# Optimization experiments

Hardware: AMD Instinct MI355X
Metric: run time of the kernel (lower is better)

## Reference

```python
import jax, jax.numpy as jnp
import numpy as np

B, N, K = 4, 4096, 16
C_IN = 128
EPS = 1e-5


def setup_inputs() -> dict:
    key = jax.random.key(0)
    ks = jax.random.split(key, 8)
    c0 = 2 * C_IN + 3  # concat channels: pos_diff(3) + feat2(128) + feat1(128)
    return {
        "pos1": jax.random.normal(ks[0], (B, 3, N), jnp.float32),
        "pos2": jax.random.normal(ks[1], (B, 3, N), jnp.float32),
        "feature1": jax.random.normal(ks[2], (B, C_IN, N), jnp.float32),
        "feature2": jax.random.normal(ks[3], (B, C_IN, N), jnp.float32),
        "W0": jax.random.normal(ks[4], (128, c0), jnp.float32) * 0.05,
        "W1": jax.random.normal(ks[5], (128, 128), jnp.float32) * 0.05,
        "W2": jax.random.normal(ks[6], (128, 128), jnp.float32) * 0.05,
        "g0": jnp.ones((128,), jnp.float32),
        "g1": jnp.ones((128,), jnp.float32),
        "g2": jnp.ones((128,), jnp.float32),
        "b0": jnp.zeros((128,), jnp.float32),
        "b1": jnp.zeros((128,), jnp.float32),
        "b2": jnp.zeros((128,), jnp.float32),
    }


def _knn_idx(pos1, pos2, k):
    # pos1, pos2: (B, 3, N).  For each point in pos1, k nearest points in pos2.
    p1 = pos1.transpose(0, 2, 1)  # (B, N, 3)
    p2 = pos2.transpose(0, 2, 1)  # (B, M, 3)
    d = (jnp.sum(p1 * p1, -1, keepdims=True)
         + jnp.sum(p2 * p2, -1)[:, None, :]
         - 2.0 * jnp.einsum("bnc,bmc->bnm", p1, p2))  # (B, N, M) squared dists
    _, idx = jax.lax.top_k(-d, k)  # (B, N, K)
    return idx


def _group(x, idx):
    # x: (B, C, M), idx: (B, N, K) -> (B, C, N, K)
    xt = x.transpose(0, 2, 1)  # (B, M, C)
    g = jax.vmap(lambda a, i: a[i])(xt, idx)  # (B, N, K, C)
    return g.transpose(0, 3, 1, 2)


def _conv_bn_relu(x, W, g, b):
    # 1x1 conv (no bias) + BatchNorm2d (training: batch stats, biased var) + ReLU
    y = jnp.einsum("oc,bcnk->bonk", W, x)
    mu = jnp.mean(y, axis=(0, 2, 3), keepdims=True)
    var = jnp.var(y, axis=(0, 2, 3), keepdims=True)
    yn = (y - mu) * jax.lax.rsqrt(var + EPS)
    return jax.nn.relu(yn * g[None, :, None, None] + b[None, :, None, None])


def reference(pos1, pos2, feature1, feature2, W0, W1, W2, g0, g1, g2, b0, b1, b2):
    idx = _knn_idx(pos1, pos2, K)                      # (B, N, K)
    pos2_g = _group(pos2, idx)                         # (B, 3, N, K)
    pos_diff = pos2_g - pos1[:, :, :, None]
    feat2_g = _group(feature2, idx)                    # (B, C, N, K)
    feat1_rep = jnp.broadcast_to(feature1[:, :, :, None], (B, C_IN, N, K))
    x = jnp.concatenate([pos_diff, feat2_g, feat1_rep], axis=1)  # (B, 2C+3, N, K)
    x = _conv_bn_relu(x, W0, g0, b0)
    x = _conv_bn_relu(x, W1, g1, b1)
    x = _conv_bn_relu(x, W2, g2, b2)
    feat1_new = jnp.max(x, axis=-1)                    # (B, mlp[-1], N)
    return (pos1, feat1_new)
```

## Files before the change

kernel.cpp:

```cpp
#include <hip/hip_runtime.h>

#define B_ 4
#define N_ 4096
#define K_ 16
#define C_ 128
#define NQ (B_*N_)
#define COLS_TOT (NQ*K_)
#define CNT_F 262144.0f
#define EPS_ 1e-5f

typedef __attribute__((ext_vector_type(8))) short short8;
typedef __attribute__((ext_vector_type(4))) float f4;
typedef __attribute__((ext_vector_type(4))) int i4;
typedef unsigned long long u64;

__device__ __forceinline__ unsigned short f2bf(float f){
  unsigned u = __builtin_bit_cast(unsigned, f);
  u = u + 0x7fffu + ((u >> 16) & 1u);
  return (unsigned short)(u >> 16);
}
__device__ __forceinline__ float bf2f(unsigned short h){
  return __builtin_bit_cast(float, ((unsigned)h) << 16);
}
__device__ __forceinline__ int swzc(int c){ return c ^ ((c >> 3) & 7); }

__global__ __launch_bounds__(256) void wconv(
    const float* __restrict__ W0, const float* __restrict__ W1, const float* __restrict__ W2,
    unsigned short* __restrict__ W0b, unsigned short* __restrict__ W0c,
    unsigned short* __restrict__ W1b, unsigned short* __restrict__ W2b)
{
  int i = blockIdx.x * 256 + threadIdx.x;
  int sel = i >> 14, r = i & 16383;
  int o = r >> 7, c = r & 127;
  float v; unsigned short* dst;
  if (sel == 0)      { v = W0[o*259 + 3   + c]; dst = W0b; }
  else if (sel == 1) { v = W0[o*259 + 131 + c]; dst = W0c; }
  else if (sel == 2) { v = W1[o*128 + c];       dst = W1b; }
  else               { v = W2[o*128 + c];       dst = W2b; }
  dst[r] = f2bf(v);
}

__global__ __launch_bounds__(256) void knn_chunk(
    const float* __restrict__ pos1, const float* __restrict__ pos2,
    u64* __restrict__ kout)
{
  __shared__ __align__(16) float pts[256*4];
  int bx = blockIdx.x;
  int b = bx >> 8, rest = bx & 255, ngrp = rest >> 4, chunk = rest & 15;
  int t = threadIdx.x;
  int m0 = chunk * 256;
  const float* p2 = pos2 + (size_t)b*3*N_;
  {
    int m = m0 + t;
    float x = p2[m], y = p2[N_ + m], z = p2[2*N_ + m];
    float sq = __fadd_rn(__fadd_rn(__fmul_rn(x,x), __fmul_rn(y,y)), __fmul_rn(z,z));
    f4 v; v.x = x; v.y = y; v.z = z; v.w = sq;
    *(f4*)(pts + t*4) = v;
  }
  __syncthreads();

  int n = ngrp*256 + t;
  const float* p1 = pos1 + (size_t)b*3*N_;
  float qx = p1[n], qy = p1[N_ + n], qz = p1[2*N_ + n];
  float qs = __fadd_rn(__fadd_rn(__fmul_rn(qx,qx), __fmul_rn(qy,qy)), __fmul_rn(qz,qz));

  u64 list[16];
  #pragma unroll
  for (int j = 0; j < 16; ++j) list[j] = ~0ull;

  #pragma unroll 1
  for (int tile = 0; tile < 16; ++tile){
    u64 tk[16];
    #pragma unroll
    for (int e = 0; e < 16; ++e){
      int it = tile*16 + e;
      f4 c = *(const f4*)(pts + it*4);
      float dot = __builtin_fmaf(qz, c.z,
                    __builtin_fmaf(qy, c.y, __fmul_rn(qx, c.x)));
      float d = __fsub_rn(__fadd_rn(qs, c.w), __fmul_rn(2.0f, dot));
      d = __fadd_rn(d, 0.0f);
      unsigned u = __builtin_bit_cast(unsigned, d);
      u ^= (unsigned)((int)u >> 31) | 0x80000000u;
      tk[e] = ((u64)u << 12) | (unsigned)(m0 + it);
    }
    #pragma unroll
    for (int k = 2; k <= 16; k <<= 1)
      #pragma unroll
      for (int j2 = k >> 1; j2 > 0; j2 >>= 1)
        #pragma unroll
        for (int i = 0; i < 16; ++i){
          int l = i ^ j2;
          if (l > i){
            bool up = ((i & k) == 0);
            u64 a = tk[i], bb = tk[l];
            bool sw = up ? (a > bb) : (a < bb);
            u64 lo = sw ? bb : a, hi = sw ? a : bb;
            tk[i] = lo; tk[l] = hi;
          }
        }
    u64 m16[16];
    #pragma unroll
    for (int i = 0; i < 16; ++i){
      u64 a = list[i], bb = tk[15 - i];
      m16[i] = a < bb ? a : bb;
    }
    #pragma unroll
    for (int j2 = 8; j2 > 0; j2 >>= 1)
      #pragma unroll
      for (int i = 0; i < 16; ++i){
        int l = i ^ j2;
        if (l > i){
          u64 a = m16[i], bb = m16[l];
          bool sw = a > bb;
          m16[i] = sw ? bb : a; m16[l] = sw ? a : bb;
        }
      }
    #pragma unroll
    for (int i = 0; i < 16; ++i) list[i] = m16[i];
  }

  int q = b*N_ + n;
  #pragma unroll
  for (int j = 0; j < 16; ++j)
    kout[(size_t)(chunk*16 + j)*NQ + q] = list[j];
}

__global__ __launch_bounds__(256) void knn_merge(
    const u64* __restrict__ kin, int* __restrict__ idxout)
{
  int q = blockIdx.x*256 + threadIdx.x;
  u64 list[16];
  #pragma unroll
  for (int j = 0; j < 16; ++j) list[j] = ~0ull;
  #pragma unroll 1
  for (int l = 0; l < 16; ++l){
    u64 lv[16];
    #pragma unroll
    for (int j = 0; j < 16; ++j)
      lv[j] = kin[(size_t)(l*16 + j)*NQ + q];
    bool dead = false;
    #pragma unroll
    for (int j = 0; j < 16; ++j){
      bool ins = !dead && (list[15] > lv[j]);
      dead = !ins;
      if (__any(ins)){
        if (ins){
          u64 key = lv[j];
          bool cm = list[14] > key;
          list[15] = cm ? list[14] : key;
          #pragma unroll
          for (int jj = 14; jj >= 1; --jj){
            bool cj = cm;
            cm = list[jj-1] > key;
            list[jj] = cj ? (cm ? list[jj-1] : key) : list[jj];
          }
          list[0] = cm ? key : list[0];
        }
      }
    }
  }
  #pragma unroll
  for (int j = 0; j < 4; ++j){
    i4 v;
    v.x = (int)(list[j*4]   & 0xFFF); v.y = (int)(list[j*4+1] & 0xFFF);
    v.z = (int)(list[j*4+2] & 0xFFF); v.w = (int)(list[j*4+3] & 0xFFF);
    *(i4*)(idxout + (size_t)q*16 + j*4) = v;
  }
}

__global__ __launch_bounds__(256) void p1_gemm(
    const float* __restrict__ feat2, const float* __restrict__ feat1,
    const unsigned short* __restrict__ W0b, const unsigned short* __restrict__ W0c,
    float* __restrict__ F2t, float* __restrict__ PREt)
{
  __shared__ __align__(16) unsigned short X[16*128*8];
  int bid = blockIdx.x;
  int sel = bid >> 7;
  const float* src = sel ? feat1 : feat2;
  const unsigned short* W = sel ? W0c : W0b;
  float* dst = sel ? PREt : F2t;
  int c0 = (bid & 127) * 128;
  int b = c0 >> 12, mm0 = c0 & 4095;
  int t = threadIdx.x;
  {
    int colt = t & 127, chh = t >> 7;
    #pragma unroll 4
    for (int it = 0; it < 64; ++it){
      int ch = it*2 + chh;
      float v = src[((size_t)b*C_ + ch)*N_ + mm0 + colt];
      X[(ch >> 3)*1024 + swzc(colt)*8 + (ch & 7)] = f2bf(v);
    }
  }
  int lane = t & 63, w = t >> 6;
  int or0 = (w >> 1)*64, c0w = (w & 1)*64;
  int lr = lane & 15, lg = lane >> 4;
  short8 af[4][4];
  #pragma unroll
  for (int ks = 0; ks < 4; ++ks)
    #pragma unroll
    for (int i = 0; i < 4; ++i)
      af[ks][i] = *(const short8*)(W + (or0 + 16*i + lr)*128 + ks*32 + 8*lg);
  __syncthreads();

  f4 acc[4][4] = {};
  #pragma unroll
  for (int ks = 0; ks < 4; ++ks){
    short8 bfr[4];
    #pragma unroll
    for (int j = 0; j < 4; ++j)
      bfr[j] = *(const short8*)(X + (ks*4 + lg)*1024 + swzc(c0w + 16*j + lr)*8);
    #pragma unroll
    for (int i = 0; i < 4; ++i)
      #pragma unroll
      for (int j = 0; j < 4; ++j)
        acc[i][j] = __builtin_amdgcn_mfma_f32_16x16x32_bf16(af[ks][i], bfr[j], acc[i][j], 0, 0, 0);
  }
  #pragma unroll
  for (int i = 0; i < 4; ++i)
    #pragma unroll
    for (int j = 0; j < 4; ++j){
      int col = c0 + c0w + 16*j + lr;
      *(f4*)(dst + (size_t)col*C_ + or0 + 16*i + 4*lg) = acc[i][j];
    }
}

__global__ __launch_bounds__(256) void k3_stats(
    const float* __restrict__ pos1, const float* __restrict__ pos2,
    const float* __restrict__ W0, const int* __restrict__ idx,
    const float* __restrict__ F2t, const float* __restrict__ PREt,
    float* __restrict__ partials)
{
  __shared__ float w0a[384];
  __shared__ float ldsS[256];
  int t = threadIdx.x;
  for (int i = t; i < 384; i += 256) w0a[i] = W0[(i/3)*259 + (i%3)];
  __syncthreads();
  int cloc = t & 15, chg = t >> 4, ch0 = chg*8;
  float wx[8], wy[8], wz[8];
  #pragma unroll
  for (int e = 0; e < 8; ++e){
    wx[e] = w0a[(ch0+e)*3]; wy[e] = w0a[(ch0+e)*3+1]; wz[e] = w0a[(ch0+e)*3+2];
  }
  float s1[8] = {}, s2[8] = {};
  int base = blockIdx.x * 256;
  for (int it = 0; it < 16; ++it){
    int col = base + it*16 + cloc;
    int nabs = col >> 4;
    int b = nabs >> 12, n = nabs & 4095;
    int m = idx[col];
    float dx = pos2[(size_t)(b*3+0)*N_ + m] - pos1[(size_t)(b*3+0)*N_ + n];
    float dy = pos2[(size_t)(b*3+1)*N_ + m] - pos1[(size_t)(b*3+1)*N_ + n];
    float dz = pos2[(size_t)(b*3+2)*N_ + m] - pos1[(size_t)(b*3+2)*N_ + n];
    const float* f2 = F2t  + ((size_t)b*N_ + m)*C_ + ch0;
    const float* pr = PREt + ((size_t)b*N_ + n)*C_ + ch0;
    #pragma unroll
    for (int e = 0; e < 8; ++e){
      float y = f2[e] + pr[e];
      y = fmaf(wx[e], dx, y); y = fmaf(wy[e], dy, y); y = fmaf(wz[e], dz, y);
      s1[e] += y; s2[e] = fmaf(y, y, s2[e]);
    }
  }
  #pragma unroll
  for (int e = 0; e < 8; ++e){
    float a = s1[e], q = s2[e];
    #pragma unroll
    for (int sft = 1; sft < 16; sft <<= 1){ a += __shfl_xor(a, sft); q += __shfl_xor(q, sft); }
    if (cloc == 0){ ldsS[ch0 + e] = a; ldsS[128 + ch0 + e] = q; }
  }
  __syncthreads();
  partials[(size_t)blockIdx.x*256 + t] = ldsS[t];
}

__global__ __launch_bounds__(256) void reduce1(const float* __restrict__ partials,
                                               float* __restrict__ partial2)
{
  int t = threadIdx.x, r0 = blockIdx.x*32;
  float a = 0.f;
  #pragma unroll 4
  for (int i = 0; i < 32; ++i) a += partials[(size_t)(r0+i)*256 + t];
  partial2[(size_t)blockIdx.x*256 + t] = a;
}

__global__ __launch_bounds__(256) void finalize(const float* __restrict__ partial2, int rows,
    const float* __restrict__ g, const float* __restrict__ bb,
    float* __restrict__ cA, float* __restrict__ cB)
{
  __shared__ float sh[256];
  int t = threadIdx.x;
  float a = 0.f;
  for (int i = 0; i < rows; ++i) a += partial2[(size_t)i*256 + t];
  sh[t] = a;
  __syncthreads();
  if (t < 128){
    float mu = sh[t] / CNT_F;
    float var = sh[128 + t] / CNT_F - mu*mu;
    float A = g[t] * rsqrtf(var + EPS_);
    cA[t] = A; cB[t] = bb[t] - mu*A;
  }
}

__global__ __launch_bounds__(256,2) void layer1_fused(
    const float* __restrict__ pos1, const float* __restrict__ pos2,
    const float* __restrict__ W0, const int* __restrict__ idx,
    const float* __restrict__ F2t, const float* __restrict__ PREt,
    unsigned short* __restrict__ ybuf,
    const unsigned short* __restrict__ Wbf,
    const float* __restrict__ cA, const float* __restrict__ cB,
    float* __restrict__ partials)
{
  __shared__ __align__(16) char lds[40960];
  unsigned short* X = (unsigned short*)lds;
  float* ldsA = (float*)(lds + 32768);
  float* ldsB = ldsA + 128;
  float* w0a  = ldsB + 128;
  float* ldsS = w0a + 384;
  int t = threadIdx.x;
  int c0 = blockIdx.x * 128;
  if (t < 128){ ldsA[t] = cA[t]; ldsB[t] = cB[t]; }
  for (int i = t; i < 384; i += 256) w0a[i] = W0[(i/3)*259 + (i%3)];
  ldsS[t] = 0.f; ldsS[256 + t] = 0.f;
  __syncthreads();

  int lane = t & 63, w = t >> 6;
  int or0 = (w >> 1)*64, c0w = (w & 1)*64;
  int lr = lane & 15, lg = lane >> 4;

  {
    int colL = t >> 1, half = t & 1;
    int col = c0 + colL;
    int nabs = col >> 4;
    int b = nabs >> 12, n = nabs & 4095;
    int m = idx[col];
    float dx = pos2[(size_t)(b*3+0)*N_ + m] - pos1[(size_t)(b*3+0)*N_ + n];
    float dy = pos2[(size_t)(b*3+1)*N_ + m] - pos1[(size_t)(b*3+1)*N_ + n];
    float dz = pos2[(size_t)(b*3+2)*N_ + m] - pos1[(size_t)(b*3+2)*N_ + n];
    const float* f2 = F2t  + ((size_t)b*N_ + m)*C_ + half*64;
    const float* pr = PREt + ((size_t)b*N_ + n)*C_ + half*64;
    int sc = swzc(colL);
    #pragma unroll
    for (int cc = 0; cc < 8; ++cc){
      int ch0 = half*64 + cc*8;
      f4 a0 = *(const f4*)(f2 + cc*8), a1 = *(const f4*)(f2 + cc*8 + 4);
      f4 b0 = *(const f4*)(pr + cc*8), b1 = *(const f4*)(pr + cc*8 + 4);
      short8 xv;
      #pragma unroll
      for (int e = 0; e < 8; ++e){
        int ch = ch0 + e;
        float fv = (e < 4 ? a0[e] : a1[e-4]);
        float pv = (e < 4 ? b0[e] : b1[e-4]);
        float y = fv + pv;
        y = fmaf(w0a[ch*3], dx, y); y = fmaf(w0a[ch*3+1], dy, y); y = fmaf(w0a[ch*3+2], dz, y);
        float v = fmaf(y, ldsA[ch], ldsB[ch]);
        v = v > 0.f ? v : 0.f;
        xv[e] = (short)f2bf(v);
      }
      *(short8*)(X + (ch0 >> 3)*1024 + sc*8) = xv;
    }
  }

  short8 af[4][4];
  #pragma unroll
  for (int ks = 0; ks < 4; ++ks)
    #pragma unroll
    for (int i = 0; i < 4; ++i)
      af[ks][i] = *(const short8*)(Wbf + (or0 + 16*i + lr)*128 + ks*32 + 8*lg);
  __syncthreads();

  f4 acc[4][4] = {};
  #pragma unroll
  for (int ks = 0; ks < 4; ++ks){
    short8 bfr[4];
    #pragma unroll
    for (int j = 0; j < 4; ++j)
      bfr[j] = *(const short8*)(X + (ks*4 + lg)*1024 + swzc(c0w + 16*j + lr)*8);
    #pragma unroll
    for (int i = 0; i < 4; ++i)
      #pragma unroll
      for (int j = 0; j < 4; ++j)
        acc[i][j] = __builtin_amdgcn_mfma_f32_16x16x32_bf16(af[ks][i], bfr[j], acc[i][j], 0, 0, 0);
  }

  #pragma unroll
  for (int i = 0; i < 4; ++i)
    #pragma unroll
    for (int e = 0; e < 4; ++e){
      float a0 = acc[i][0][e], a1 = acc[i][1][e], a2 = acc[i][2][e], a3 = acc[i][3][e];
      float s1 = (a0 + a1) + (a2 + a3);
      float s2 = (a0*a0 + a1*a1) + (a2*a2 + a3*a3);
      #pragma unroll
      for (int sft = 1; sft < 16; sft <<= 1){ s1 += __shfl_xor(s1, sft); s2 += __shfl_xor(s2, sft); }
      if (lr == 0){
        int o = or0 + 16*i + 4*lg + e;
        ldsS[(w & 1)*256 + o] = s1;
        ldsS[(w & 1)*256 + 128 + o] = s2;
      }
    }

  __syncthreads();
  unsigned short* OT = (unsigned short*)lds;
  #pragma unroll
  for (int i = 0; i < 4; ++i)
    #pragma unroll
    for (int j = 0; j < 4; ++j){
      int col = c0w + 16*j + lr;
      int o0 = or0 + 16*i + 4*lg;
      unsigned long long pv =
          (unsigned long long)f2bf(acc[i][j][0])
        | ((unsigned long long)f2bf(acc[i][j][1]) << 16)
        | ((unsigned long long)f2bf(acc[i][j][2]) << 32)
        | ((unsigned long long)f2bf(acc[i][j][3]) << 48);
      *(unsigned long long*)(OT + col*136 + o0) = pv;
    }
  __syncthreads();
  {
    int colL = t >> 1, half = t & 1;
    unsigned short* dst = ybuf + (size_t)(c0 + colL)*128 + half*64;
    #pragma unroll
    for (int cc = 0; cc < 8; ++cc){
      short8 v = *(const short8*)(OT + colL*136 + half*64 + cc*8);
      *(short8*)(dst + cc*8) = v;
    }
  }
  __syncthreads();
  partials[(size_t)blockIdx.x*256 + t] = ldsS[t] + ldsS[256 + t];
}

__global__ __launch_bounds__(256,2) void layer_gemm_last(
    unsigned short* ybuf,
    const unsigned short* __restrict__ Wbf,
    const float* __restrict__ cA, const float* __restrict__ cB,
    float* __restrict__ y2max,
    float* __restrict__ partials)
{
  __shared__ __align__(16) char lds[38912];
  unsigned short* X = (unsigned short*)lds;
  float* ldsA = (float*)(lds + 34816);
  float* ldsB = ldsA + 128;
  float* ldsS = ldsB + 128;
  int t = threadIdx.x;
  int c0 = blockIdx.x * 128;
  if (t < 128){ ldsA[t] = cA[t]; ldsB[t] = cB[t]; }
  ldsS[t] = 0.f; ldsS[256 + t] = 0.f;

  int lane = t & 63, w = t >> 6;
  int or0 = (w >> 1)*64, c0w = (w & 1)*64;
  int lr = lane & 15, lg = lane >> 4;
  short8 af[4][4];
  #pragma unroll
  for (int ks = 0; ks < 4; ++ks)
    #pragma unroll
    for (int i = 0; i < 4; ++i)
      af[ks][i] = *(const short8*)(Wbf + (or0 + 16*i + lr)*128 + ks*32 + 8*lg);
  __syncthreads();

  {
    int colL = t >> 1, half = t & 1;
    const unsigned short* src = ybuf + (size_t)(c0 + colL)*128 + half*64;
    int sc = swzc(colL);
    #pragma unroll
    for (int cc = 0; cc < 8; ++cc){
      int ch0 = half*64 + cc*8;
      short8 yv = *(const short8*)(src + cc*8);
      short8 xv;
      #pragma unroll
      for (int e = 0; e < 8; ++e){
        float f = bf2f((unsigned short)yv[e]);
        float v = fmaf(f, ldsA[ch0 + e], ldsB[ch0 + e]);
        v = v > 0.f ? v : 0.f;
        xv[e] = (short)f2bf(v);
      }
      *(short8*)(X + (ch0 >> 3)*1024 + sc*8) = xv;
    }
  }
  __syncthreads();

  f4 acc[4][4] = {};
  #pragma unroll
  for (int ks = 0; ks < 4; ++ks){
    short8 bfr[4];
    #pragma unroll
    for (int j = 0; j < 4; ++j)
      bfr[j] = *(const short8*)(X + (ks*4 + lg)*1024 + swzc(c0w + 16*j + lr)*8);
    #pragma unroll
    for (int i = 0; i < 4; ++i)
      #pragma unroll
      for (int j = 0; j < 4; ++j)
        acc[i][j] = __builtin_amdgcn_mfma_f32_16x16x32_bf16(af[ks][i], bfr[j], acc[i][j], 0, 0, 0);
  }

  #pragma unroll
  for (int i = 0; i < 4; ++i)
    #pragma unroll
    for (int e = 0; e < 4; ++e){
      float a0 = acc[i][0][e], a1 = acc[i][1][e], a2 = acc[i][2][e], a3 = acc[i][3][e];
      float s1 = (a0 + a1) + (a2 + a3);
      float s2 = (a0*a0 + a1*a1) + (a2*a2 + a3*a3);
      #pragma unroll
      for (int sft = 1; sft < 16; sft <<= 1){ s1 += __shfl_xor(s1, sft); s2 += __shfl_xor(s2, sft); }
      if (lr == 0){
        int o = or0 + 16*i + 4*lg + e;
        ldsS[(w & 1)*256 + o] = s1;
        ldsS[(w & 1)*256 + 128 + o] = s2;
      }
    }

  float keep[4][4] = {};
  #pragma unroll
  for (int j = 0; j < 4; ++j)
    #pragma unroll
    for (int i = 0; i < 4; ++i)
      #pragma unroll
      for (int e = 0; e < 4; ++e){
        float v = acc[i][j][e];
        #pragma unroll
        for (int sft = 1; sft < 16; sft <<= 1) v = fmaxf(v, __shfl_xor(v, sft));
        if (lr == j) keep[i][e] = v;
      }
  if (lr < 4){
    int colg = c0 + c0w + 16*lr;
    int nabs = colg >> 4;
    float* dst = y2max + (size_t)nabs*C_;
    #pragma unroll
    for (int i = 0; i < 4; ++i){
      f4 v; v.x = keep[i][0]; v.y = keep[i][1]; v.z = keep[i][2]; v.w = keep[i][3];
      *(f4*)(dst + or0 + 16*i + 4*lg) = v;
    }
  }
  __syncthreads();
  partials[(size_t)blockIdx.x*256 + t] = ldsS[t] + ldsS[256 + t];
}

__global__ __launch_bounds__(256) void k7_out(
    const float* __restrict__ y2max, const float* __restrict__ cA,
    const float* __restrict__ cB, float* __restrict__ outF)
{
  __shared__ __align__(16) float T[128*65];
  int t = threadIdx.x, bid = blockIdx.x;
  int b = bid >> 6, n0 = (bid & 63)*64;
  {
    int nl = t >> 2, o0 = (t & 3)*32;
    const float* src = y2max + ((size_t)b*N_ + n0 + nl)*C_ + o0;
    #pragma unroll
    for (int jj = 0; jj < 8; ++jj){
      f4 v = *(const f4*)(src + jj*4);
      T[(o0 + jj*4 + 0)*65 + nl] = v.x;
      T[(o0 + jj*4 + 1)*65 + nl] = v.y;
      T[(o0 + jj*4 + 2)*65 + nl] = v.z;
      T[(o0 + jj*4 + 3)*65 + nl] = v.w;
    }
  }
  __syncthreads();
  {
    int o = t >> 1, half = t & 1;
    float A = cA[o], Bb = cB[o];
    float* dst = outF + ((size_t)b*C_ + o)*N_ + n0 + half*32;
    #pragma unroll
    for (int jj = 0; jj < 8; ++jj){
      f4 v;
      float x0 = fmaf(T[o*65 + half*32 + jj*4+0], A, Bb);
      float x1 = fmaf(T[o*65 + half*32 + jj*4+1], A, Bb);
      float x2 = fmaf(T[o*65 + half*32 + jj*4+2], A, Bb);
      float x3 = fmaf(T[o*65 + half*32 + jj*4+3], A, Bb);
      v.x = x0 > 0.f ? x0 : 0.f; v.y = x1 > 0.f ? x1 : 0.f;
      v.z = x2 > 0.f ? x2 : 0.f; v.w = x3 > 0.f ? x3 : 0.f;
      *(f4*)(dst + jj*4) = v;
    }
  }
}

extern "C" void kernel_launch(void* const* d_in, const int* in_sizes, int n_in,
                              void* d_out, int out_size, void* d_ws, size_t ws_size,
                              hipStream_t stream)
{
  (void)in_sizes; (void)n_in; (void)out_size; (void)ws_size;
  const float* pos1  = (const float*)d_in[0];
  const float* pos2  = (const float*)d_in[1];
  const float* feat1 = (const float*)d_in[2];
  const float* feat2 = (const float*)d_in[3];
  const float* W0 = (const float*)d_in[4];
  const float* W1 = (const float*)d_in[5];
  const float* W2 = (const float*)d_in[6];
  const float* g0 = (const float*)d_in[7];
  const float* g1 = (const float*)d_in[8];
  const float* g2 = (const float*)d_in[9];
  const float* b0 = (const float*)d_in[10];
  const float* b1 = (const float*)d_in[11];
  const float* b2 = (const float*)d_in[12];

  char* ws = (char*)d_ws;
  size_t off = 0;
  auto alloc = [&](size_t bytes){ size_t r = off; off += (bytes + 255) & ~(size_t)255; return r; };
  int*   idx     = (int*)  (ws + alloc((size_t)COLS_TOT*4));
  float* F2t     = (float*)(ws + alloc((size_t)NQ*C_*4));
  float* PREt    = (float*)(ws + alloc((size_t)NQ*C_*4));
  unsigned short* ybuf = (unsigned short*)(ws + alloc((size_t)COLS_TOT*C_*2));
  float* y2max   = (float*)(ws + alloc((size_t)NQ*C_*4));
  float* partials= (float*)(ws + alloc((size_t)2048*256*4));
  float* partial2= (float*)(ws + alloc((size_t)64*256*4));
  float* coef    = (float*)(ws + alloc((size_t)6*128*4));
  unsigned short* W0bb = (unsigned short*)(ws + alloc(16384*2));
  unsigned short* W0cb = (unsigned short*)(ws + alloc(16384*2));
  unsigned short* W1b  = (unsigned short*)(ws + alloc(16384*2));
  unsigned short* W2b  = (unsigned short*)(ws + alloc(16384*2));

  u64* knn_k = (u64*)ybuf;

  float* cA0 = coef,       *cB0 = coef + 128;
  float* cA1 = coef + 256, *cB1 = coef + 384;
  float* cA2 = coef + 512, *cB2 = coef + 640;

  wconv<<<256, 256, 0, stream>>>(W0, W1, W2, W0bb, W0cb, W1b, W2b);
  knn_chunk<<<1024, 256, 0, stream>>>(pos1, pos2, knn_k);
  knn_merge<<<64, 256, 0, stream>>>(knn_k, idx);
  p1_gemm<<<256, 256, 0, stream>>>(feat2, feat1, W0bb, W0cb, F2t, PREt);
  k3_stats<<<1024, 256, 0, stream>>>(pos1, pos2, W0, idx, F2t, PREt, partials);
  reduce1<<<32, 256, 0, stream>>>(partials, partial2);
  finalize<<<1, 256, 0, stream>>>(partial2, 32, g0, b0, cA0, cB0);
  layer1_fused<<<2048, 256, 0, stream>>>(pos1, pos2, W0, idx, F2t, PREt,
                                          ybuf, W1b, cA0, cB0, partials);
  reduce1<<<64, 256, 0, stream>>>(partials, partial2);
  finalize<<<1, 256, 0, stream>>>(partial2, 64, g1, b1, cA1, cB1);
  layer_gemm_last<<<2048, 256, 0, stream>>>(ybuf, W2b, cA1, cB1, y2max, partials);
  reduce1<<<64, 256, 0, stream>>>(partials, partial2);
  finalize<<<1, 256, 0, stream>>>(partial2, 64, g2, b2, cA2, cB2);
  k7_out<<<256, 256, 0, stream>>>(y2max, cA2, cB2, (float*)d_out + (size_t)B_*3*N_);
  hipMemcpyAsync(d_out, d_in[0], (size_t)B_*3*N_*4, hipMemcpyDeviceToDevice, stream);
}
```

Measured before the change: 365.2 us.

## Merge small kernels and fold BN stat finalize into a last-block reduction

Packs independent small kernels into shared launches by giving them separate block ranges. Weight conversion joins the KNN chunk kernel, KNN merge joins the first feature GEMM, and the pos1 output copy joins the final output kernel instead of using a separate memcpy. The separate reduce and finalize launches for each BatchNorm layer become one kernel: an atomic counter picks the last block, which finishes the reduction and resets the counter. This removes several launches and serial gaps, at the cost of adding a memset, atomics and threadfences, and it relies on the counter being reset correctly between calls.

```diff
diff --git a/kernel.cpp b/kernel.cpp
--- a/kernel.cpp
+++ b/kernel.cpp
@@ -24,26 +24,26 @@
 }
 __device__ __forceinline__ int swzc(int c){ return c ^ ((c >> 3) & 7); }
 
-__global__ __launch_bounds__(256) void wconv(
-    const float* __restrict__ W0, const float* __restrict__ W1, const float* __restrict__ W2,
+__global__ __launch_bounds__(256) void knn_wconv(
+    const float* __restrict__ pos1, const float* __restrict__ pos2,
+    u64* __restrict__ kout,
+    const float* __restrict__ W0, const float* __restrict__ W1,
+    const float* __restrict__ W2,
     unsigned short* __restrict__ W0b, unsigned short* __restrict__ W0c,
     unsigned short* __restrict__ W1b, unsigned short* __restrict__ W2b)
 {
-  int i = blockIdx.x * 256 + threadIdx.x;
-  int sel = i >> 14, r = i & 16383;
-  int o = r >> 7, c = r & 127;
-  float v; unsigned short* dst;
-  if (sel == 0)      { v = W0[o*259 + 3   + c]; dst = W0b; }
-  else if (sel == 1) { v = W0[o*259 + 131 + c]; dst = W0c; }
-  else if (sel == 2) { v = W1[o*128 + c];       dst = W1b; }
-  else               { v = W2[o*128 + c];       dst = W2b; }
-  dst[r] = f2bf(v);
-}
-
-__global__ __launch_bounds__(256) void knn_chunk(
-    const float* __restrict__ pos1, const float* __restrict__ pos2,
-    u64* __restrict__ kout)
-{
+  if (blockIdx.x >= 1024){
+    int i = (blockIdx.x - 1024) * 256 + threadIdx.x;
+    int sel = i >> 14, r = i & 16383;
+    int o = r >> 7, c = r & 127;
+    float v; unsigned short* dst;
+    if (sel == 0)      { v = W0[o*259 + 3   + c]; dst = W0b; }
+    else if (sel == 1) { v = W0[o*259 + 131 + c]; dst = W0c; }
+    else if (sel == 2) { v = W1[o*128 + c];       dst = W1b; }
+    else               { v = W2[o*128 + c];       dst = W2b; }
+    dst[r] = f2bf(v);
+    return;
+  }
   __shared__ __align__(16) float pts[256*4];
   int bx = blockIdx.x;
   int b = bx >> 8, rest = bx & 255, ngrp = rest >> 4, chunk = rest & 15;
@@ -81,7 +81,7 @@
       d = __fadd_rn(d, 0.0f);
       unsigned u = __builtin_bit_cast(unsigned, d);
       u ^= (unsigned)((int)u >> 31) | 0x80000000u;
-      tk[e] = ((u64)u << 12) | (unsigned)(m0 + it);
+      tk[e] = ((u64)u << 32) | (unsigned)(m0 + it);
     }
     #pragma unroll
     for (int k = 2; k <= 16; k <<= 1)
@@ -125,56 +125,55 @@
     kout[(size_t)(chunk*16 + j)*NQ + q] = list[j];
 }
 
-__global__ __launch_bounds__(256) void knn_merge(
-    const u64* __restrict__ kin, int* __restrict__ idxout)
-{
-  int q = blockIdx.x*256 + threadIdx.x;
-  u64 list[16];
-  #pragma unroll
-  for (int j = 0; j < 16; ++j) list[j] = ~0ull;
-  #pragma unroll 1
-  for (int l = 0; l < 16; ++l){
-    u64 lv[16];
-    #pragma unroll
-    for (int j = 0; j < 16; ++j)
-      lv[j] = kin[(size_t)(l*16 + j)*NQ + q];
-    bool dead = false;
-    #pragma unroll
-    for (int j = 0; j < 16; ++j){
-      bool ins = !dead && (list[15] > lv[j]);
-      dead = !ins;
-      if (__any(ins)){
-        if (ins){
-          u64 key = lv[j];
-          bool cm = list[14] > key;
-          list[15] = cm ? list[14] : key;
-          #pragma unroll
-          for (int jj = 14; jj >= 1; --jj){
-            bool cj = cm;
-            cm = list[jj-1] > key;
-            list[jj] = cj ? (cm ? list[jj-1] : key) : list[jj];
-          }
-          list[0] = cm ? key : list[0];
-        }
-      }
-    }
-  }
-  #pragma unroll
-  for (int j = 0; j < 4; ++j){
-    i4 v;
-    v.x = (int)(list[j*4]   & 0xFFF); v.y = (int)(list[j*4+1] & 0xFFF);
-    v.z = (int)(list[j*4+2] & 0xFFF); v.w = (int)(list[j*4+3] & 0xFFF);
-    *(i4*)(idxout + (size_t)q*16 + j*4) = v;
-  }
-}
-
-__global__ __launch_bounds__(256) void p1_gemm(
+__global__ __launch_bounds__(256) void merge_p1(
+    const u64* __restrict__ kin, int* __restrict__ idxout,
     const float* __restrict__ feat2, const float* __restrict__ feat1,
     const unsigned short* __restrict__ W0b, const unsigned short* __restrict__ W0c,
     float* __restrict__ F2t, float* __restrict__ PREt)
 {
+  if (blockIdx.x < 64){
+    int q = blockIdx.x*256 + threadIdx.x;
+    u64 list[16];
+    #pragma unroll
+    for (int j = 0; j < 16; ++j) list[j] = ~0ull;
+    #pragma unroll 1
+    for (int l = 0; l < 16; ++l){
+      u64 lv[16];
+      #pragma unroll
+      for (int j = 0; j < 16; ++j)
+        lv[j] = kin[(size_t)(l*16 + j)*NQ + q];
+      bool dead = false;
+      #pragma unroll
+      for (int j = 0; j < 16; ++j){
+        bool ins = !dead && (list[15] > lv[j]);
+        dead = !ins;
+        if (__any(ins)){
+          if (ins){
+            u64 key = lv[j];
+            bool cm = list[14] > key;
+            list[15] = cm ? list[14] : key;
+            #pragma unroll
+            for (int jj = 14; jj >= 1; --jj){
+              bool cj = cm;
+              cm = list[jj-1] > key;
+              list[jj] = cj ? (cm ? list[jj-1] : key) : list[jj];
+            }
+            list[0] = cm ? key : list[0];
+          }
+        }
+      }
+    }
+    #pragma unroll
+    for (int j = 0; j < 4; ++j){
+      i4 v;
+      v.x = (int)(list[j*4]   & 0xFFF); v.y = (int)(list[j*4+1] & 0xFFF);
+      v.z = (int)(list[j*4+2] & 0xFFF); v.w = (int)(list[j*4+3] & 0xFFF);
+      *(i4*)(idxout + (size_t)q*16 + j*4) = v;
+    }
+    return;
+  }
   __shared__ __align__(16) unsigned short X[16*128*8];
-  int bid = blockIdx.x;
+  int bid = blockIdx.x - 64;
   int sel = bid >> 7;
   const float* src = sel ? feat1 : feat2;
   const unsigned short* W = sel ? W0c : W0b;
@@ -271,25 +270,31 @@
   partials[(size_t)blockIdx.x*256 + t] = ldsS[t];
 }
 
-__global__ __launch_bounds__(256) void reduce1(const float* __restrict__ partials,
-                                               float* __restrict__ partial2)
-{
-  int t = threadIdx.x, r0 = blockIdx.x*32;
+__global__ __launch_bounds__(256) void redfin(
+    const float* __restrict__ partials, float* __restrict__ partial2,
+    const float* __restrict__ g, const float* __restrict__ bb,
+    float* __restrict__ cA, float* __restrict__ cB,
+    int* __restrict__ counter)
+{
+  __shared__ float sh[256];
+  __shared__ int isLast;
+  int t = threadIdx.x, blk = blockIdx.x, R = gridDim.x;
   float a = 0.f;
+  int r0 = blk*32;
   #pragma unroll 4
   for (int i = 0; i < 32; ++i) a += partials[(size_t)(r0+i)*256 + t];
-  partial2[(size_t)blockIdx.x*256 + t] = a;
-}
-
-__global__ __launch_bounds__(256) void finalize(const float* __restrict__ partial2, int rows,
-    const float* __restrict__ g, const float* __restrict__ bb,
-    float* __restrict__ cA, float* __restrict__ cB)
-{
-  __shared__ float sh[256];
-  int t = threadIdx.x;
-  float a = 0.f;
-  for (int i = 0; i < rows; ++i) a += partial2[(size_t)i*256 + t];
-  sh[t] = a;
+  partial2[(size_t)blk*256 + t] = a;
+  __threadfence();
+  if (t == 0){
+    int old = atomicAdd(counter, 1);
+    isLast = (old == R - 1);
+  }
+  __syncthreads();
+  if (!isLast) return;
+  __threadfence();
+  float s = 0.f;
+  for (int i = 0; i < R; ++i) s += partial2[(size_t)i*256 + t];
+  sh[t] = s;
   __syncthreads();
   if (t < 128){
     float mu = sh[t] / CNT_F;
@@ -297,6 +302,7 @@
     float A = g[t] * rsqrtf(var + EPS_);
     cA[t] = A; cB[t] = bb[t] - mu*A;
   }
+  if (t == 0) *counter = 0;
 }
 
 __global__ __launch_bounds__(256,2) void layer1_fused(
@@ -530,10 +536,16 @@
   partials[(size_t)blockIdx.x*256 + t] = ldsS[t] + ldsS[256 + t];
 }
 
-__global__ __launch_bounds__(256) void k7_out(
+__global__ __launch_bounds__(256) void k7_fat(
     const float* __restrict__ y2max, const float* __restrict__ cA,
-    const float* __restrict__ cB, float* __restrict__ outF)
-{
+    const float* __restrict__ cB, float* __restrict__ outF,
+    const float* __restrict__ pos1, float* __restrict__ out0)
+{
+  if (blockIdx.x >= 256){
+    int i = ((blockIdx.x - 256)*256 + threadIdx.x)*4;
+    *(f4*)(out0 + i) = *(const f4*)(pos1 + i);
+    return;
+  }
   __shared__ __align__(16) float T[128*65];
   int t = threadIdx.x, bid = blockIdx.x;
   int b = bid >> 6, n0 = (bid & 63)*64;
@@ -598,6 +610,7 @@
   float* partials= (float*)(ws + alloc((size_t)2048*256*4));
   float* partial2= (float*)(ws + alloc((size_t)64*256*4));
   float* coef    = (float*)(ws + alloc((size_t)6*128*4));
+  int*   ctrs    = (int*)  (ws + alloc(256));
   unsigned short* W0bb = (unsigned short*)(ws + alloc(16384*2));
   unsigned short* W0cb = (unsigned short*)(ws + alloc(16384*2));
   unsigned short* W1b  = (unsigned short*)(ws + alloc(16384*2));
@@ -609,20 +622,17 @@
   float* cA1 = coef + 256, *cB1 = coef + 384;
   float* cA2 = coef + 512, *cB2 = coef + 640;
 
-  wconv<<<256, 256, 0, stream>>>(W0, W1, W2, W0bb, W0cb, W1b, W2b);
-  knn_chunk<<<1024, 256, 0, stream>>>(pos1, pos2, knn_k);
-  knn_merge<<<64, 256, 0, stream>>>(knn_k, idx);
-  p1_gemm<<<256, 256, 0, stream>>>(feat2, feat1, W0bb, W0cb, F2t, PREt);
+  hipMemsetAsync(ctrs, 0, 256, stream);
+  knn_wconv<<<1280, 256, 0, stream>>>(pos1, pos2, knn_k, W0, W1, W2,
+                                       W0bb, W0cb, W1b, W2b);
+  merge_p1<<<320, 256, 0, stream>>>(knn_k, idx, feat2, feat1, W0bb, W0cb, F2t, PREt);
   k3_stats<<<1024, 256, 0, stream>>>(pos1, pos2, W0, idx, F2t, PREt, partials);
-  reduce1<<<32, 256, 0, stream>>>(partials, partial2);
-  finalize<<<1, 256, 0, stream>>>(partial2, 32, g0, b0, cA0, cB0);
+  redfin<<<32, 256, 0, stream>>>(partials, partial2, g0, b0, cA0, cB0, ctrs + 0);
   layer1_fused<<<2048, 256, 0, stream>>>(pos1, pos2, W0, idx, F2t, PREt,
                                           ybuf, W1b, cA0, cB0, partials);
-  reduce1<<<64, 256, 0, stream>>>(partials, partial2);
-  finalize<<<1, 256, 0, stream>>>(partial2, 64, g1, b1, cA1, cB1);
+  redfin<<<64, 256, 0, stream>>>(partials, partial2, g1, b1, cA1, cB1, ctrs + 16);
   layer_gemm_last<<<2048, 256, 0, stream>>>(ybuf, W2b, cA1, cB1, y2max, partials);
-  reduce1<<<64, 256, 0, stream>>>(partials, partial2);
-  finalize<<<1, 256, 0, stream>>>(partial2, 64, g2, b2, cA2, cB2);
-  k7_out<<<256, 256, 0, stream>>>(y2max, cA2, cB2, (float*)d_out + (size_t)B_*3*N_);
-  hipMemcpyAsync(d_out, d_in[0], (size_t)B_*3*N_*4, hipMemcpyDeviceToDevice, stream);
-}
+  redfin<<<64, 256, 0, stream>>>(partials, partial2, g2, b2, cA2, cB2, ctrs + 32);
+  k7_fat<<<304, 256, 0, stream>>>(y2max, cA2, cB2,
+                                   (float*)d_out + (size_t)B_*3*N_, pos1, (float*)d_out);
+}
```

Result: no change. 361.4 us (median of 2 runs) (-1.1%).
